# Performance work log

Measured on AMD Instinct MI355X. Metric: run time of the kernel, lower is better.

The kernel has to match this reference:

```python
import jax, jax.numpy as jnp
import numpy as np
import math

HEAVY = 128
RECENT = 128
NUM_HEADS = 32
HEAD_DIM = 64
ROPE_THETA = 10000.0


def _rope(x, pos):
    # x: (B, h, S, D); Falcon rotate_half RoPE
    d = x.shape[-1]
    inv = 1.0 / (ROPE_THETA ** (jnp.arange(0, d, 2, dtype=jnp.float32) / d))
    freqs = pos[:, None].astype(jnp.float32) * inv[None, :]          # (S, d/2)
    emb = jnp.concatenate([freqs, freqs], axis=-1)                   # (S, d)
    cos, sin = jnp.cos(emb), jnp.sin(emb)
    x1, x2 = x[..., : d // 2], x[..., d // 2:]
    return x * cos + jnp.concatenate([-x2, x1], axis=-1) * sin


def _heavy_hitter_mask(scores, heavy, recent):
    # H2O 'local nonoverlap' heavy-hitter mask, shared across heads (MQA).
    # scores: (B, H, S, S) -> bool mask (B, 1, S, S)
    B, H, S, _ = scores.shape
    probs = jax.nn.softmax(scores.astype(jnp.float32), axis=-1).sum(axis=1, keepdims=True)  # (B,1,S,S)
    start = heavy + recent
    col = jnp.arange(S)
    acc0 = jnp.where(col[None, None, :] < start,
                     probs[:, :, :start, :].sum(axis=2), 0.0)        # (B,1,S)
    NEG = jnp.float32(-1e30)

    def step(acc, t):
        row = jnp.take(probs, t, axis=2)                             # (B,1,S)
        # heavy candidates: accumulated scores strictly before the recent window
        cand = jnp.where(col[None, None, :] < t - recent, acc, NEG)
        _, idx = jax.lax.top_k(cand, heavy)                          # (B,1,heavy)
        heavy_m = (col[None, None, None, :] == idx[..., None]).any(axis=-2)  # (B,1,S)
        recent_m = (col >= t - recent) & (col <= t)
        row_mask = heavy_m | recent_m[None, None, :]
        acc = (acc + row * row_mask) * row_mask                      # keep only selected keys
        return acc, row_mask

    _, rows = jax.lax.scan(step, acc0, jnp.arange(start, S))         # (S-start, B, 1, S)
    rows = jnp.moveaxis(rows, 0, 2)                                  # (B, 1, S-start, S)
    init = jnp.broadcast_to((col < start)[None, None, None, :], (B, 1, start, S))
    return jnp.concatenate([init, rows], axis=2)


def setup_inputs() -> dict:
    key = jax.random.key(0)
    k1, k2, k3 = jax.random.split(key, 3)
    B, S, Hdim = 1, 2048, NUM_HEADS * HEAD_DIM
    hidden_states = jax.random.normal(k1, (B, S, Hdim), dtype=jnp.float32)
    w_qkv = jax.random.normal(k2, ((NUM_HEADS + 2) * HEAD_DIM, Hdim), dtype=jnp.float32) * (Hdim ** -0.5)
    w_dense = jax.random.normal(k3, (Hdim, Hdim), dtype=jnp.float32) * (Hdim ** -0.5)
    return {"hidden_states": hidden_states, "w_qkv": w_qkv, "w_dense": w_dense}


def reference(hidden_states, w_qkv, w_dense):
    B, S, Hdim = hidden_states.shape
    H, D = NUM_HEADS, HEAD_DIM
    fused = (hidden_states @ w_qkv.T).reshape(B, S, H + 2, D)        # MQA split
    q = jnp.swapaxes(fused[:, :, :H], 1, 2)                          # (B,H,S,D)
    k = jnp.swapaxes(fused[:, :, H:H + 1], 1, 2)                     # (B,1,S,D)
    v = jnp.swapaxes(fused[:, :, H + 1:], 1, 2)                      # (B,1,S,D)
    pos = jnp.arange(S)
    q = _rope(q, pos)
    k = _rope(k, pos)
    scores = jnp.einsum('bhqd,bokd->bhqk', q, k) / math.sqrt(D)      # (B,H,S,S)
    mask = _heavy_hitter_mask(scores, HEAVY, RECENT)                 # (B,1,S,S)
    r = jnp.arange(S)
    recent_win = r[None, :] >= (r[:, None] - RECENT)                 # triu(diag=-RECENT)
    causal = r[None, :] <= r[:, None]                                # tril(diag=0)
    mask = (mask | recent_win[None, None]) & causal[None, None]
    neg = jnp.finfo(scores.dtype).min
    probs = jax.nn.softmax(jnp.where(mask, scores, neg).astype(jnp.float32), axis=-1).astype(scores.dtype)
    out = jnp.einsum('bhqk,bokd->bhqd', probs, v)                    # (B,H,S,D)
    out = jnp.swapaxes(out, 1, 2).reshape(B, S, H * D)
    return out @ w_dense.T
```

## Files before the change

### kernel.cpp

```cpp
#include <hip/hip_runtime.h>
#include <hip/hip_bf16.h>
#include <cstdint>

#define S 2048
#define NH 32
#define HD 64
#define NJ 34
#define FUSED_N (NJ * HD)
#define HDIM (NH * HD)
#define HEAVY_K 128
#define RECENT_W 128
#define START_T 256

typedef __attribute__((ext_vector_type(8))) short short8;
typedef __attribute__((ext_vector_type(4))) float floatx4;

static __device__ __forceinline__ unsigned short f2bf(float f) {
    unsigned u = __float_as_uint(f);
    unsigned r = (u + 0x7FFF + ((u >> 16) & 1)) >> 16;
    return (unsigned short)r;
}
static __device__ __forceinline__ float bf2f(unsigned short b) {
    return __uint_as_float(((unsigned)b) << 16);
}

#define GBM 128
#define GBN 128
#define GBK 32
__global__ __launch_bounds__(256) void gemm_nt_mfma(const float* __restrict__ A,
                                                    const float* __restrict__ B,
                                                    float* __restrict__ C,
                                                    int M, int N, int K)
{
    __shared__ unsigned short Ash[GBM][GBK + 8], Asl[GBM][GBK + 8];
    __shared__ unsigned short Bsh[GBN][GBK + 8], Bsl[GBN][GBK + 8];
    const int bm = blockIdx.y * GBM;
    const int bn = blockIdx.x * GBN;
    const int tid = threadIdx.x;
    const int w = tid >> 6, lane = tid & 63;
    const int rsub = lane & 15;
    const int d0 = (lane >> 4) * 8;

    floatx4 acc[2][8] = {};

    for (int k0 = 0; k0 < K; k0 += GBK) {
#pragma unroll
        for (int i = 0; i < 4; ++i) {
            int l = tid + i * 256;
            int r = l >> 3;
            int kq = (l & 7) * 4;
            float4 xa = *(const float4*)&A[(size_t)(bm + r) * K + k0 + kq];
            float4 xb = *(const float4*)&B[(size_t)(bn + r) * K + k0 + kq];
            ushort4 ah, al, bh, bl;
            ah.x = f2bf(xa.x); al.x = f2bf(xa.x - bf2f(ah.x));
            ah.y = f2bf(xa.y); al.y = f2bf(xa.y - bf2f(ah.y));
            ah.z = f2bf(xa.z); al.z = f2bf(xa.z - bf2f(ah.z));
            ah.w = f2bf(xa.w); al.w = f2bf(xa.w - bf2f(ah.w));
            bh.x = f2bf(xb.x); bl.x = f2bf(xb.x - bf2f(bh.x));
            bh.y = f2bf(xb.y); bl.y = f2bf(xb.y - bf2f(bh.y));
            bh.z = f2bf(xb.z); bl.z = f2bf(xb.z - bf2f(bh.z));
            bh.w = f2bf(xb.w); bl.w = f2bf(xb.w - bf2f(bh.w));
            *(ushort4*)&Ash[r][kq] = ah;
            *(ushort4*)&Asl[r][kq] = al;
            *(ushort4*)&Bsh[r][kq] = bh;
            *(ushort4*)&Bsl[r][kq] = bl;
        }
        __syncthreads();

        short8 a_h[2], a_l[2];
#pragma unroll
        for (int mt = 0; mt < 2; ++mt) {
            const int row = w * 32 + mt * 16 + rsub;
            a_h[mt] = *(const short8*)&Ash[row][d0];
            a_l[mt] = *(const short8*)&Asl[row][d0];
        }
#pragma unroll
        for (int nt = 0; nt < 8; ++nt) {
            const int col = nt * 16 + rsub;
            short8 b_h = *(const short8*)&Bsh[col][d0];
            short8 b_l = *(const short8*)&Bsl[col][d0];
#pragma unroll
            for (int mt = 0; mt < 2; ++mt) {
                acc[mt][nt] = __builtin_amdgcn_mfma_f32_16x16x32_bf16(a_l[mt], b_h, acc[mt][nt], 0, 0, 0);
                acc[mt][nt] = __builtin_amdgcn_mfma_f32_16x16x32_bf16(a_h[mt], b_l, acc[mt][nt], 0, 0, 0);
                acc[mt][nt] = __builtin_amdgcn_mfma_f32_16x16x32_bf16(a_h[mt], b_h, acc[mt][nt], 0, 0, 0);
            }
        }
        __syncthreads();
    }
#pragma unroll
    for (int mt = 0; mt < 2; ++mt) {
        const int orow = bm + w * 32 + mt * 16 + (lane >> 4) * 4;
#pragma unroll
        for (int nt = 0; nt < 8; ++nt) {
            const int ocol = bn + nt * 16 + rsub;
#pragma unroll
            for (int r = 0; r < 4; ++r)
                C[(size_t)(orow + r) * N + ocol] = acc[mt][nt][r];
        }
    }
}

__global__ __launch_bounds__(256) void rope_split_kernel(const float* __restrict__ fused,
                                                         unsigned short* __restrict__ qb,
                                                         unsigned short* __restrict__ kb,
                                                         float* __restrict__ v)
{
    int idx = blockIdx.x * 256 + threadIdx.x;
    const int total = S * NJ * HD;
    if (idx >= total) return;
    int t = idx / FUSED_N;
    int rem = idx - t * FUSED_N;
    int j = rem >> 6;
    int d = rem & 63;
    float x = fused[idx];
    if (j == 33) { v[t * HD + d] = x; return; }
    int i = d & 31;
    double inv = exp2(-(double)i * (13.287712379549449 / 32.0));
    double ang = (double)t * inv;
    float c  = (float)cos(ang);
    float sn = (float)sin(ang);
    float xo = fused[idx - d + ((d < 32) ? (d + 32) : (d - 32))];
    float rot = (d < 32) ? -xo : xo;
    unsigned short outv = f2bf(x * c + rot * sn);
    if (j == 32) kb[t * HD + d] = outv;
    else         qb[(size_t)t * HDIM + j * HD + d] = outv;
}

__global__ __launch_bounds__(256) void z_kernel(const unsigned short* __restrict__ qb,
                                                const unsigned short* __restrict__ kb,
                                                float* __restrict__ zinv)
{
    const int t0 = blockIdx.x * 32;
    const int h  = blockIdx.y;
    const int w    = threadIdx.x >> 6;
    const int lane = threadIdx.x & 63;
    const int rsub = lane & 15;
    const int d0   = (lane >> 4) * 8;
    __shared__ float zl[4][32];

    short8 a[2][2];
#pragma unroll
    for (int mt = 0; mt < 2; ++mt) {
        const short8* ap = (const short8*)(qb + (size_t)(t0 + mt * 16 + rsub) * HDIM + h * HD + d0);
        a[mt][0] = ap[0];
        a[mt][1] = ap[4];
    }
    float z[2][4] = {};
    for (int nt = 0; nt < 32; ++nt) {
        const int c = w * 512 + nt * 16 + rsub;
        const short8* bp = (const short8*)(kb + (size_t)c * HD + d0);
        short8 b0 = bp[0];
        short8 b1 = bp[4];
#pragma unroll
        for (int mt = 0; mt < 2; ++mt) {
            floatx4 acc = {0.f, 0.f, 0.f, 0.f};
            acc = __builtin_amdgcn_mfma_f32_16x16x32_bf16(a[mt][0], b0, acc, 0, 0, 0);
            acc = __builtin_amdgcn_mfma_f32_16x16x32_bf16(a[mt][1], b1, acc, 0, 0, 0);
#pragma unroll
            for (int r = 0; r < 4; ++r) z[mt][r] += __expf(acc[r] * 0.125f);
        }
    }
#pragma unroll
    for (int mt = 0; mt < 2; ++mt)
#pragma unroll
        for (int r = 0; r < 4; ++r) {
            float zz = z[mt][r];
#pragma unroll
            for (int off = 1; off < 16; off <<= 1) zz += __shfl_xor(zz, off);
            z[mt][r] = zz;
        }
    if (rsub == 0) {
#pragma unroll
        for (int mt = 0; mt < 2; ++mt)
#pragma unroll
            for (int r = 0; r < 4; ++r)
                zl[w][mt * 16 + (lane >> 4) * 4 + r] = z[mt][r];
    }
    __syncthreads();
    if (threadIdx.x < 32) {
        float s = zl[0][threadIdx.x] + zl[1][threadIdx.x] + zl[2][threadIdx.x] + zl[3][threadIdx.x];
        zinv[(size_t)(t0 + threadIdx.x) * NH + h] = 1.0f / s;
    }
}

__global__ __launch_bounds__(256) void pnorm_kernel(const unsigned short* __restrict__ qb,
                                                    const unsigned short* __restrict__ kb,
                                                    const float* __restrict__ zinv,
                                                    float* __restrict__ P)
{
    const int t0 = blockIdx.y * 32;
    const int cb = blockIdx.x * 256;
    const int w    = threadIdx.x >> 6;
    const int lane = threadIdx.x & 63;
    const int rsub = lane & 15;
    const int d0   = (lane >> 4) * 8;
    __shared__ float zi[32][33];
    for (int i = threadIdx.x; i < 32 * 32; i += 256) {
        int row = i >> 5, hh = i & 31;
        zi[row][hh] = zinv[(size_t)(t0 + row) * NH + hh];
    }
    __syncthreads();

    float pacc[2][4][4] = {};
    for (int h = 0; h < NH; ++h) {
        short8 a[2][2];
#pragma unroll
        for (int mt = 0; mt < 2; ++mt) {
            const short8* ap = (const short8*)(qb + (size_t)(t0 + mt * 16 + rsub) * HDIM + h * HD + d0);
            a[mt][0] = ap[0];
            a[mt][1] = ap[4];
        }
        float zv[2][4];
#pragma unroll
        for (int mt = 0; mt < 2; ++mt)
#pragma unroll
            for (int r = 0; r < 4; ++r)
                zv[mt][r] = zi[mt * 16 + (lane >> 4) * 4 + r][h];
#pragma unroll
        for (int nt = 0; nt < 4; ++nt) {
            const int c = cb + w * 64 + nt * 16 + rsub;
            const short8* bp = (const short8*)(kb + (size_t)c * HD + d0);
            short8 b0 = bp[0];
            short8 b1 = bp[4];
#pragma unroll
            for (int mt = 0; mt < 2; ++mt) {
                floatx4 acc = {0.f, 0.f, 0.f, 0.f};
                acc = __builtin_amdgcn_mfma_f32_16x16x32_bf16(a[mt][0], b0, acc, 0, 0, 0);
                acc = __builtin_amdgcn_mfma_f32_16x16x32_bf16(a[mt][1], b1, acc, 0, 0, 0);
#pragma unroll
                for (int r = 0; r < 4; ++r)
                    pacc[mt][nt][r] += __expf(acc[r] * 0.125f) * zv[mt][r];
            }
        }
    }
#pragma unroll
    for (int mt = 0; mt < 2; ++mt)
#pragma unroll
        for (int nt = 0; nt < 4; ++nt)
#pragma unroll
            for (int r = 0; r < 4; ++r) {
                int row = t0 + mt * 16 + (lane >> 4) * 4 + r;
                int col = cb + w * 64 + nt * 16 + rsub;
                P[(size_t)row * S + col] = pacc[mt][nt][r];
            }
}

__global__ __launch_bounds__(256) void acc_init_kernel(const float* __restrict__ P,
                                                       float* __restrict__ acc_init)
{
    int c = blockIdx.x * 256 + threadIdx.x;
    float s = 0.f;
    if (c < 256) {
        const float* p = P + c;
        float s0 = 0.f, s1 = 0.f, s2 = 0.f, s3 = 0.f;
#pragma unroll 4
        for (int t = 0; t < 256; t += 4) {
            s0 += p[(size_t)t * S];
            s1 += p[(size_t)(t + 1) * S];
            s2 += p[(size_t)(t + 2) * S];
            s3 += p[(size_t)(t + 3) * S];
        }
        s = (s0 + s1) + (s2 + s3);
    }
    if (c <= 256) s += P[(size_t)256 * S + c];
    acc_init[c] = s;
}

template <int CTRL>
static __device__ __forceinline__ unsigned dppmin(unsigned x)
{
    int t = __builtin_amdgcn_update_dpp((int)x, (int)x, CTRL, 0xf, 0xf, false);
    unsigned u = (unsigned)t;
    return x < u ? x : u;
}

__global__ void scan_kernel(const float* __restrict__ P,
                            const float* __restrict__ acc_init,
                            unsigned short* __restrict__ heavy)
{
    __shared__ float accL[S];
    const int lane = threadIdx.x;

    for (int c = lane; c < S; c += 64) accL[c] = acc_init[c];

    heavy[START_T * HEAVY_K + lane] = (unsigned short)lane;
    heavy[START_T * HEAVY_K + 64 + lane] = (unsigned short)(lane + 64);

    int   c0 = lane, c1 = lane + 64;
    float v0 = acc_init[lane], v1 = acc_init[lane + 64];

    float A0p, A1p, AXp, SR0p, SR1p, STp, SNp;
    {
        const float* Pn = P + (size_t)257 * S;
        A0p  = Pn[c0];
        A1p  = Pn[c1];
        AXp  = Pn[127];
        SR0p = Pn[129 + lane];
        SR1p = Pn[193 + lane];
        STp  = Pn[257];
        SNp  = Pn[128];
    }
    float AR0p = accL[129 + lane];
    float AR1p = accL[193 + lane];
    float nvp  = acc_init[128];
    bool e0p = false, e1p = false;

    for (int t = START_T + 1; t < S; ++t) {
        const int tn = (t + 1 < S) ? (t + 1) : (S - 1);
        const float* Pn = P + (size_t)tn * S;
        float nA0  = Pn[c0];
        float nA1  = Pn[c1];
        float nAX  = Pn[tn - 130];
        float nSR0 = Pn[tn - 128 + lane];
        float nSR1 = Pn[tn - 64 + lane];
        float nST  = Pn[tn];
        float nSN  = Pn[tn - 129];

        unsigned b0 = __float_as_uint(v0), b1 = __float_as_uint(v1);
        unsigned xv = b0 < b1 ? b0 : b1;
        xv = dppmin<0x111>(xv);
        xv = dppmin<0x112>(xv);
        xv = dppmin<0x114>(xv);
        xv = dppmin<0x118>(xv);
        unsigned r15 = (unsigned)__builtin_amdgcn_readlane((int)xv, 15);
        unsigned r31 = (unsigned)__builtin_amdgcn_readlane((int)xv, 31);
        unsigned r47 = (unsigned)__builtin_amdgcn_readlane((int)xv, 47);
        unsigned r63 = (unsigned)__builtin_amdgcn_readlane((int)xv, 63);
        unsigned ma = r15 < r31 ? r15 : r31;
        unsigned mb = r47 < r63 ? r47 : r63;
        unsigned mvb = ma < mb ? ma : mb;

        unsigned long long m0 = __ballot(b0 == mvb);
        unsigned long long m1 = __ballot(b1 == mvb);
        int mc;
        if (__popcll(m0) + __popcll(m1) == 1) {
            mc = m0 ? __builtin_amdgcn_readlane(c0, __ffsll((unsigned long long)m0) - 1)
                    : __builtin_amdgcn_readlane(c1, __ffsll((unsigned long long)m1) - 1);
        } else {
            unsigned long long p0 = ((unsigned long long)b0 << 32) | (unsigned)(~c0);
            unsigned long long p1 = ((unsigned long long)b1 << 32) | (unsigned)(~c1);
            unsigned long long mm = p1 < p0 ? p1 : p0;
#pragma unroll
            for (int off = 1; off < 64; off <<= 1) {
                unsigned long long om = __shfl_xor(mm, off);
                if (om < mm) mm = om;
            }
            mc = (int)(~(unsigned)mm);
        }

        const int newc = t - 129;
        const bool evict = mvb < __float_as_uint(nvp);
        float pv0 = e0p ? AXp : A0p;
        float pv1 = e1p ? AXp : A1p;
        bool e0 = evict && (c0 == mc);
        bool e1 = evict && (c1 == mc);
        v0 = e0 ? (nvp + SNp) : (v0 + pv0);
        c0 = e0 ? newc : c0;
        v1 = e1 ? (nvp + SNp) : (v1 + pv1);
        c1 = e1 ? newc : c1;

        heavy[(size_t)t * HEAVY_K + lane]      = (unsigned short)c0;
        heavy[(size_t)t * HEAVY_K + 64 + lane] = (unsigned short)c1;

        float w0 = AR0p + SR0p;
        float w1 = AR1p + SR1p;
        accL[t - 128 + lane] = w0;
        accL[t - 64 + lane]  = w1;
        if (lane == 0) accL[t] = STp;

        nvp = __uint_as_float((unsigned)__builtin_amdgcn_readlane((int)__float_as_uint(w0), 0));

        AR0p = accL[tn - 128 + lane];
        AR1p = accL[tn - 64 + lane];

        A0p = nA0; A1p = nA1; AXp = nAX;
        SR0p = nSR0; SR1p = nSR1; STp = nST; SNp = nSN;
        e0p = e0; e1p = e1;
    }
}

__global__ __launch_bounds__(256) void attn_kernel(const unsigned short* __restrict__ qb,
                                                   const unsigned short* __restrict__ kb,
                                                   const float* __restrict__ v,
                                                   const unsigned short* __restrict__ heavy,
                                                   float* __restrict__ attn)
{
    const int t = blockIdx.x;
    const int tid = threadIdx.x;
    __shared__ float qs[HDIM];
    __shared__ float sc[NH][258];
    __shared__ unsigned short cols[260];
    __shared__ float zpart[NH][8];
    __shared__ float zf[NH];
    const int cnt = (t < START_T) ? (t + 1) : 257;
    {
        const short8* qr = (const short8*)(qb + (size_t)t * HDIM);
        short8 qv = qr[tid];
#pragma unroll
        for (int j = 0; j < 8; ++j) qs[tid * 8 + j] = bf2f((unsigned short)qv[j]);
    }
    if (t < START_T) {
        for (int j = tid; j < cnt; j += 256) cols[j] = (unsigned short)j;
    } else {
        if (tid < 128) cols[tid] = heavy[(size_t)t * HEAVY_K + tid];
        else           cols[tid] = (unsigned short)(t - 256 + tid);
        if (tid == 0)  cols[256] = (unsigned short)t;
    }
    __syncthreads();
    {
        const int h = tid & 31;
        const float* qh = qs + h * HD;
        for (int j = tid >> 5; j < cnt; j += 8) {
            const short8* kc8 = (const short8*)(kb + (size_t)cols[j] * HD);
            float s = 0.f;
#pragma unroll
            for (int dq = 0; dq < 8; ++dq) {
                short8 kv = kc8[dq];
#pragma unroll
                for (int e = 0; e < 8; ++e)
                    s += qh[dq * 8 + e] * bf2f((unsigned short)kv[e]);
            }
            sc[h][j] = s * 0.125f;
        }
    }
    __syncthreads();
    {
        const int h2 = tid >> 3, sub = tid & 7;
        float z = 0.f;
        for (int j = sub; j < cnt; j += 8) {
            float e = __expf(sc[h2][j]);
            sc[h2][j] = e;
            z += e;
        }
        zpart[h2][sub] = z;
    }
    __syncthreads();
    if (tid < NH) {
        float z = 0.f;
#pragma unroll
        for (int s2 = 0; s2 < 8; ++s2) z += zpart[tid][s2];
        zf[tid] = 1.0f / z;
    }
    __syncthreads();
    {
        const int h2 = tid >> 3;
        const int dbase = (tid & 7) * 8;
        float o[8] = {0, 0, 0, 0, 0, 0, 0, 0};
        for (int j = 0; j < cnt; ++j) {
            float p = sc[h2][j];
            const float* vc = v + (size_t)cols[j] * HD + dbase;
            float4 va = *(const float4*)vc;
            float4 vb = *(const float4*)(vc + 4);
            o[0] += p * va.x; o[1] += p * va.y; o[2] += p * va.z; o[3] += p * va.w;
            o[4] += p * vb.x; o[5] += p * vb.y; o[6] += p * vb.z; o[7] += p * vb.w;
        }
        float zi = zf[h2];
        float* op = attn + (size_t)t * HDIM + h2 * HD + dbase;
        float4 ra = make_float4(o[0] * zi, o[1] * zi, o[2] * zi, o[3] * zi);
        float4 rb = make_float4(o[4] * zi, o[5] * zi, o[6] * zi, o[7] * zi);
        *(float4*)op = ra;
        *(float4*)(op + 4) = rb;
    }
}

extern "C" void kernel_launch(void* const* d_in, const int* in_sizes, int n_in,
                              void* d_out, int out_size, void* d_ws, size_t ws_size,
                              hipStream_t stream)
{
    (void)in_sizes; (void)n_in; (void)out_size; (void)ws_size;
    const float* hs      = (const float*)d_in[0];
    const float* w_qkv   = (const float*)d_in[1];
    const float* w_dense = (const float*)d_in[2];
    float* out = (float*)d_out;
    char* ws = (char*)d_ws;

    float* fused = (float*)(ws);
    float* P     = (float*)(ws);
    float* attn  = (float*)(ws);
    unsigned short* qb = (unsigned short*)(ws + 17825792);
    unsigned short* kb = (unsigned short*)(ws + 26214400);
    float* v           = (float*)(ws + 26476544);
    float* zinv        = (float*)(ws + 27000832);
    unsigned short* heavy = (unsigned short*)(ws + 27262976);
    float* acc_init       = (float*)(ws + 27787264);

    dim3 g1(FUSED_N / GBN, S / GBM);
    gemm_nt_mfma<<<g1, 256, 0, stream>>>(hs, w_qkv, fused, S, FUSED_N, HDIM);

    int total = S * NJ * HD;
    rope_split_kernel<<<(total + 255) / 256, 256, 0, stream>>>(fused, qb, kb, v);

    dim3 gz(S / 32, NH);
    z_kernel<<<gz, 256, 0, stream>>>(qb, kb, zinv);

    dim3 gp(S / 256, S / 32);
    pnorm_kernel<<<gp, 256, 0, stream>>>(qb, kb, zinv, P);

    acc_init_kernel<<<S / 256, 256, 0, stream>>>(P, acc_init);

    scan_kernel<<<1, 64, 0, stream>>>(P, acc_init, heavy);

    attn_kernel<<<S, 256, 0, stream>>>(qb, kb, v, heavy, attn);

    dim3 g2(HDIM / GBN, S / GBM);
    gemm_nt_mfma<<<g2, 256, 0, stream>>>(attn, w_dense, out, S, HDIM, HDIM);
}
```

Before: 1.351 ms.

## Precompute recent-window entry values in parallel and deepen scan prefetch to two steps

A new parallel kernel precomputes, for each column, the accumulated score it will hold when it leaves the recent window (NV). This removes the per-step LDS accumulation of the whole recent window from the single-wavefront serial scan. The scan now prefetches P rows two steps ahead and tracks eviction state from the previous two steps so it can pick the correct increment. This shortens the serial critical path in exchange for an extra small kernel launch and more registers and bookkeeping in the scan.

```diff
diff --git a/kernel.cpp b/kernel.cpp
--- a/kernel.cpp
+++ b/kernel.cpp
@@ -267,6 +267,23 @@
     acc_init[c] = s;
 }
 
+__global__ __launch_bounds__(256) void nv_kernel(const float* __restrict__ P,
+                                                 const float* __restrict__ acc_init,
+                                                 float* __restrict__ NV)
+{
+    int c = 128 + blockIdx.x * 256 + threadIdx.x;
+    if (c > 1918) return;
+    float s;
+    int t0;
+    if (c <= 256) { s = acc_init[c]; t0 = 257; }
+    else          { s = P[(size_t)c * S + c]; t0 = c + 1; }
+    const int t1 = c + 128;
+    const float* p = P + c;
+    for (int t = t0; t <= t1; ++t)
+        s += p[(size_t)t * S];
+    NV[c] = s;
+}
+
 template <int CTRL>
 static __device__ __forceinline__ unsigned dppmin(unsigned x)
 {
@@ -277,12 +294,10 @@
 
 __global__ void scan_kernel(const float* __restrict__ P,
                             const float* __restrict__ acc_init,
+                            const float* __restrict__ NV,
                             unsigned short* __restrict__ heavy)
 {
-    __shared__ float accL[S];
     const int lane = threadIdx.x;
-
-    for (int c = lane; c < S; c += 64) accL[c] = acc_init[c];
 
     heavy[START_T * HEAVY_K + lane] = (unsigned short)lane;
     heavy[START_T * HEAVY_K + 64 + lane] = (unsigned short)(lane + 64);
@@ -290,32 +305,29 @@
     int   c0 = lane, c1 = lane + 64;
     float v0 = acc_init[lane], v1 = acc_init[lane + 64];
 
-    float A0p, A1p, AXp, SR0p, SR1p, STp, SNp;
-    {
-        const float* Pn = P + (size_t)257 * S;
-        A0p  = Pn[c0];
-        A1p  = Pn[c1];
-        AXp  = Pn[127];
-        SR0p = Pn[129 + lane];
-        SR1p = Pn[193 + lane];
-        STp  = Pn[257];
-        SNp  = Pn[128];
-    }
-    float AR0p = accL[129 + lane];
-    float AR1p = accL[193 + lane];
-    float nvp  = acc_init[128];
-    bool e0p = false, e1p = false;
+    const float* P257 = P + (size_t)257 * S;
+    const float* P258 = P + (size_t)258 * S;
+    float A0_t = P257[c0], A1_t = P257[c1];
+    float AX_t = 0.f, AY_t = 0.f;
+    float SN_t = P257[128];
+    float NV_t = NV[128];
+    float A0_n = P258[c0], A1_n = P258[c1];
+    float AX_n = 0.f;
+    float AY_n = P258[128];
+    float SN_n = P258[129];
+    float NV_n = NV[129];
+    bool e0_m1 = false, e1_m1 = false;
+    bool e0_m2 = false, e1_m2 = false;
 
     for (int t = START_T + 1; t < S; ++t) {
-        const int tn = (t + 1 < S) ? (t + 1) : (S - 1);
-        const float* Pn = P + (size_t)tn * S;
-        float nA0  = Pn[c0];
-        float nA1  = Pn[c1];
-        float nAX  = Pn[tn - 130];
-        float nSR0 = Pn[tn - 128 + lane];
-        float nSR1 = Pn[tn - 64 + lane];
-        float nST  = Pn[tn];
-        float nSN  = Pn[tn - 129];
+        const int t2 = (t + 2 < S) ? (t + 2) : (S - 1);
+        const float* P2 = P + (size_t)t2 * S;
+        float pA0 = P2[c0];
+        float pA1 = P2[c1];
+        float pAX = P2[t2 - 131];
+        float pAY = P2[t2 - 130];
+        float pSN = P2[t2 - 129];
+        float pNV = NV[t2 - 129];
 
         unsigned b0 = __float_as_uint(v0), b1 = __float_as_uint(v1);
         unsigned xv = b0 < b1 ? b0 : b1;
@@ -350,33 +362,25 @@
         }
 
         const int newc = t - 129;
-        const bool evict = mvb < __float_as_uint(nvp);
-        float pv0 = e0p ? AXp : A0p;
-        float pv1 = e1p ? AXp : A1p;
+        const bool evict = mvb < __float_as_uint(NV_t);
+        float pv0 = e0_m1 ? AY_t : (e0_m2 ? AX_t : A0_t);
+        float pv1 = e1_m1 ? AY_t : (e1_m2 ? AX_t : A1_t);
         bool e0 = evict && (c0 == mc);
         bool e1 = evict && (c1 == mc);
-        v0 = e0 ? (nvp + SNp) : (v0 + pv0);
+        v0 = e0 ? (NV_t + SN_t) : (v0 + pv0);
         c0 = e0 ? newc : c0;
-        v1 = e1 ? (nvp + SNp) : (v1 + pv1);
+        v1 = e1 ? (NV_t + SN_t) : (v1 + pv1);
         c1 = e1 ? newc : c1;
 
         heavy[(size_t)t * HEAVY_K + lane]      = (unsigned short)c0;
         heavy[(size_t)t * HEAVY_K + 64 + lane] = (unsigned short)c1;
 
-        float w0 = AR0p + SR0p;
-        float w1 = AR1p + SR1p;
-        accL[t - 128 + lane] = w0;
-        accL[t - 64 + lane]  = w1;
-        if (lane == 0) accL[t] = STp;
-
-        nvp = __uint_as_float((unsigned)__builtin_amdgcn_readlane((int)__float_as_uint(w0), 0));
-
-        AR0p = accL[tn - 128 + lane];
-        AR1p = accL[tn - 64 + lane];
-
-        A0p = nA0; A1p = nA1; AXp = nAX;
-        SR0p = nSR0; SR1p = nSR1; STp = nST; SNp = nSN;
-        e0p = e0; e1p = e1;
+        A0_t = A0_n; A1_t = A1_n; AX_t = AX_n; AY_t = AY_n;
+        SN_t = SN_n; NV_t = NV_n;
+        A0_n = pA0; A1_n = pA1; AX_n = pAX; AY_n = pAY;
+        SN_n = pSN; NV_n = pNV;
+        e0_m2 = e0_m1; e1_m2 = e1_m1;
+        e0_m1 = e0;   e1_m1 = e1;
     }
 }
 
@@ -484,6 +488,7 @@
     float* zinv        = (float*)(ws + 27000832);
     unsigned short* heavy = (unsigned short*)(ws + 27262976);
     float* acc_init       = (float*)(ws + 27787264);
+    float* NV             = (float*)(ws + 27795456);
 
     dim3 g1(FUSED_N / GBN, S / GBM);
     gemm_nt_mfma<<<g1, 256, 0, stream>>>(hs, w_qkv, fused, S, FUSED_N, HDIM);
@@ -499,7 +504,9 @@
 
     acc_init_kernel<<<S / 256, 256, 0, stream>>>(P, acc_init);
 
-    scan_kernel<<<1, 64, 0, stream>>>(P, acc_init, heavy);
+    nv_kernel<<<7, 256, 0, stream>>>(P, acc_init, NV);
+
+    scan_kernel<<<1, 64, 0, stream>>>(P, acc_init, NV, heavy);
 
     attn_kernel<<<S, 256, 0, stream>>>(qb, kb, v, heavy, attn);
 
```

Measured after the change: 1.403 ms. 3.8% more time.
